# Performance work log

Measured on AMD Instinct MI355X. Metric: run time of the kernel, lower is better.

Reference implementation:

```python
import jax, jax.numpy as jnp
import numpy as np

N = 50000      # nodes
E = 600000     # edges
D_IN = 128
D = 128        # embedding_size
H = 2 * D      # GENConv MLP hidden (expansion=2, num_layers=2)
L = 6          # gnn_layers
OUT = 2        # out_channels
EPS_MSG = 1e-7   # GENConv message eps
EPS_SM = 1e-16   # PyG softmax denominator eps
LN_EPS = 1e-5


def setup_inputs() -> dict:
    key = jax.random.key(0)
    ks = jax.random.split(key, 18)
    s_in = 1.0 / np.sqrt(D_IN)
    s_d = 1.0 / np.sqrt(D)
    s_h = 1.0 / np.sqrt(H)
    return {
        "x": jax.random.normal(ks[0], (N, D_IN), jnp.float32),
        "edge_index": jax.random.randint(ks[1], (2, E), 0, N, jnp.int64),
        # node encoder
        "enc_W": jax.random.normal(ks[2], (D_IN, D), jnp.float32) * s_in,
        "enc_b": jnp.zeros((D,), jnp.float32),
        # per-layer DeepGCN params (stacked over L layers)
        "ln_g": jnp.ones((L, D), jnp.float32),
        "ln_b": jnp.zeros((L, D), jnp.float32),
        "t": jnp.ones((L,), jnp.float32),  # learnable softmax temperature
        "W1": jax.random.normal(ks[3], (L, D, H), jnp.float32) * s_d,
        "b1": jnp.zeros((L, H), jnp.float32),
        "mln_g": jnp.ones((L, H), jnp.float32),
        "mln_b": jnp.zeros((L, H), jnp.float32),
        "W2": jax.random.normal(ks[4], (L, H, D), jnp.float32) * s_h,
        "b2": jnp.zeros((L, D), jnp.float32),
        # final MLP head (linear_layers=2)
        "lin_W1": jax.random.normal(ks[5], (D, D), jnp.float32) * s_d,
        "lin_b1": jnp.zeros((D,), jnp.float32),
        "lin_W2": jax.random.normal(ks[6], (D, OUT), jnp.float32) * s_d,
        "lin_b2": jnp.zeros((OUT,), jnp.float32),
    }


def _layernorm(h, g, b):
    mu = jnp.mean(h, axis=-1, keepdims=True)
    var = jnp.mean(jnp.square(h - mu), axis=-1, keepdims=True)
    return (h - mu) * jax.lax.rsqrt(var + LN_EPS) * g + b


def _genconv(h, src, dst, t, W1, b1, mg, mb, W2, b2):
    """GENConv with softmax aggregation: gather -> segment softmax -> scatter -> MLP."""
    msg = jax.nn.relu(h[src]) + EPS_MSG            # [E, D]
    scaled = msg * t
    mmax = jax.ops.segment_max(scaled, dst, num_segments=N)  # [N, D]
    mmax = jnp.where(jnp.isfinite(mmax), mmax, 0.0)          # empty segments
    ex = jnp.exp(scaled - mmax[dst])                          # [E, D]
    denom = jax.ops.segment_sum(ex, dst, num_segments=N)     # [N, D]
    alpha = ex / (denom[dst] + EPS_SM)
    agg = jax.ops.segment_sum(msg * alpha, dst, num_segments=N)  # [N, D]
    out = agg + h                                  # root/self term
    z = out @ W1 + b1                              # [N, 2D]
    z = jax.nn.relu(_layernorm(z, mg, mb))
    return z @ W2 + b2                             # [N, D]


def reference(x, edge_index, enc_W, enc_b, ln_g, ln_b, t, W1, b1,
              mln_g, mln_b, W2, b2, lin_W1, lin_b1, lin_W2, lin_b2):
    src, dst = edge_index[0], edge_index[1]
    h = x @ enc_W + enc_b                          # node encoder [N, D]
    for i in range(L):                             # DeepGCNLayer 'res+' blocks
        g = _layernorm(h, ln_g[i], ln_b[i])
        g = jax.nn.relu(g)                         # (dropout: inference no-op)
        g = _genconv(g, src, dst, t[i], W1[i], b1[i], mln_g[i], mln_b[i], W2[i], b2[i])
        h = h + g
    h = jax.nn.relu(h @ lin_W1 + lin_b1)           # head (dropout_rate=None)
    return h @ lin_W2 + lin_b2                     # [N, OUT]
```

## Files before the change

### kernel.cpp

```cpp
#include <hip/hip_runtime.h>

#define NN 50000
#define EE 600000
#define DD 128
#define HH 256
#define LL 6
#define NB 49

typedef _Float16 f16x8 __attribute__((ext_vector_type(8)));
typedef float f32x4 __attribute__((ext_vector_type(4)));

__device__ __forceinline__ float bf2f(unsigned short u){
  unsigned int x = ((unsigned int)u) << 16; float f; __builtin_memcpy(&f, &x, 4); return f;
}
__device__ __forceinline__ unsigned short f2bf(float f){
  unsigned int x; __builtin_memcpy(&x, &f, 4);
  unsigned int lsb = (x >> 16) & 1u; x += 0x7fffu + lsb; return (unsigned short)(x >> 16);
}
__device__ __forceinline__ float wave_sum(float v){
  #pragma unroll
  for (int off = 32; off >= 1; off >>= 1) v += __shfl_xor(v, off, 64);
  return v;
}
__device__ __forceinline__ unsigned short f2h(float f){
  _Float16 h = (_Float16)f; unsigned short u; __builtin_memcpy(&u, &h, 2); return u;
}
__device__ __forceinline__ float h2f(unsigned short u){
  _Float16 h; __builtin_memcpy(&h, &u, 2); return (float)h;
}

__global__ void k_detect(const unsigned short* __restrict__ xh,
                         const unsigned int* __restrict__ ew,
                         int* __restrict__ flags){
  __shared__ int s_bad, s_nz;
  int t = threadIdx.x;
  if (t == 0){ s_bad = 0; s_nz = 0; }
  __syncthreads();
  int bad = 0;
  for (int i = t; i < 512; i += 256){
    unsigned e = (xh[i] >> 7) & 0xffu;
    if (e < 96u || e > 135u) bad = 1;
  }
  if (bad) atomicOr(&s_bad, 1);
  int nz = 0;
  for (int i = t; i < 1024; i += 256)
    if ((i & 1) && ew[i] != 0u) nz = 1;
  if (nz) atomicOr(&s_nz, 1);
  __syncthreads();
  if (t == 0){
    flags[0] = s_bad ? 1 : 0;
    flags[1] = s_nz ? 0 : 1;
  }
}

__global__ void k_cvt_edges(const void* __restrict__ ei, const int* __restrict__ flags,
                            int* __restrict__ s32, int* __restrict__ d32){
  int e = blockIdx.x*256 + threadIdx.x;
  if (e >= EE) return;
  int sv, dv;
  if (flags[1]){
    const long long* p = (const long long*)ei;
    sv = (int)p[e]; dv = (int)p[EE + e];
  } else {
    const int* p = (const int*)ei;
    sv = p[e]; dv = p[EE + e];
  }
  s32[e] = ((unsigned)sv < (unsigned)NN) ? sv : 0;
  d32[e] = ((unsigned)dv < (unsigned)NN) ? dv : 0;
}

__global__ void k_hist(const int* __restrict__ dst, int* __restrict__ deg){
  int e = blockIdx.x*256 + threadIdx.x;
  if (e < EE) atomicAdd(&deg[dst[e]], 1);
}

__global__ void k_blocksum(const int* __restrict__ deg, int* __restrict__ bsum){
  __shared__ int ws[4];
  int t = threadIdx.x, b = blockIdx.x;
  int s = 0;
  int i0 = b*1024 + t*4;
  #pragma unroll
  for (int j=0;j<4;j++){ int i = i0+j; if (i < NN) s += deg[i]; }
  #pragma unroll
  for (int off=32; off>=1; off>>=1) s += __shfl_xor(s, off, 64);
  if ((t&63)==0) ws[t>>6] = s;
  __syncthreads();
  if (t==0) bsum[b] = ws[0]+ws[1]+ws[2]+ws[3];
}

__global__ void k_scanb(const int* __restrict__ bsum, int* __restrict__ boff, int* __restrict__ rowptr){
  int lane = threadIdx.x;
  int v = (lane < NB) ? bsum[lane] : 0;
  int inc = v;
  #pragma unroll
  for (int off=1; off<64; off<<=1){ int u = __shfl_up(inc, off, 64); if (lane>=off) inc += u; }
  if (lane < NB) boff[lane] = inc - v;
  if (lane == 63) rowptr[NN] = inc;
}

__global__ void k_scanscatter(const int* __restrict__ deg, const int* __restrict__ boff,
                              int* __restrict__ rowptr, int* __restrict__ pos){
  __shared__ int ws[4];
  int t = threadIdx.x, b = blockIdx.x;
  int lane = t & 63, wid = t >> 6;
  int i0 = b*1024 + t*4;
  int d[4];
  #pragma unroll
  for (int j=0;j<4;j++){ int i=i0+j; d[j] = (i<NN)? deg[i] : 0; }
  int tot = d[0]+d[1]+d[2]+d[3];
  int inc = tot;
  #pragma unroll
  for (int off=1; off<64; off<<=1){ int u = __shfl_up(inc, off, 64); if (lane>=off) inc += u; }
  if (lane==63) ws[wid] = inc;
  __syncthreads();
  int woff = 0;
  for (int w=0; w<wid; w++) woff += ws[w];
  int base = boff[b] + woff + (inc - tot);
  int pre = 0;
  #pragma unroll
  for (int j=0;j<4;j++){
    int i = i0+j;
    if (i<NN){ rowptr[i] = base + pre; pos[i] = base + pre; }
    pre += d[j];
  }
}

__global__ void k_fill(const int* __restrict__ src, const int* __restrict__ dst,
                       int* __restrict__ pos, int* __restrict__ csr){
  int e = blockIdx.x*256 + threadIdx.x;
  if (e < EE){
    int d = dst[e];
    int p = atomicAdd(&pos[d], 1);
    csr[p] = src[e];
  }
}

__global__ void k_prep_w(const int* __restrict__ flags,
    const void* __restrict__ encW, const void* __restrict__ linW1,
    const void* __restrict__ W1, const void* __restrict__ W2,
    unsigned short* __restrict__ ph, unsigned short* __restrict__ pl)
{
  int idx = blockIdx.x*256 + threadIdx.x;
  int fp32 = flags[0];
  const void* src; int off;
  if (idx < 16384){ int n=idx>>7, k=idx&127; src=encW; off=k*128+n; }
  else if (idx < 32768){ int o=idx-16384; int n=o>>7, k=o&127; src=linW1; off=k*128+n; }
  else if (idx < 229376){ int o=idx-32768; int l=o>>15, r=o&32767; int n=r>>7, k=r&127; src=W1; off=l*32768+k*256+n; }
  else { int o=idx-229376; int l=o>>15, r=o&32767; int n=r>>8, k=r&255; src=W2; off=l*32768+k*128+n; }
  float w = fp32 ? ((const float*)src)[off] : bf2f(((const unsigned short*)src)[off]);
  unsigned short h = f2h(w);
  ph[idx] = h;
  pl[idx] = f2h(w - h2f(h));
}

#define SM_ENCB 0
#define SM_LNG 128
#define SM_LNB 896
#define SM_TV 1664
#define SM_B1 1670
#define SM_MG 3206
#define SM_MB 4742
#define SM_B2 6278
#define SM_LINB1 7046
#define SM_LINW2 7174
#define SM_LINB2 7430
#define SM_TOT 7432
__global__ void k_prep_small(const int* __restrict__ flags,
    const void* s0, const void* s1, const void* s2, const void* s3,
    const void* s4, const void* s5, const void* s6, const void* s7,
    const void* s8, const void* s9, const void* s10, float* __restrict__ out)
{
  int i = blockIdx.x*256 + threadIdx.x;
  if (i >= SM_TOT) return;
  int fp32 = flags[0];
  const void* src; int off;
  if      (i < SM_LNG)  { src=s0;  off=i; }
  else if (i < SM_LNB)  { src=s1;  off=i-SM_LNG; }
  else if (i < SM_TV)   { src=s2;  off=i-SM_LNB; }
  else if (i < SM_B1)   { src=s3;  off=i-SM_TV; }
  else if (i < SM_MG)   { src=s4;  off=i-SM_B1; }
  else if (i < SM_MB)   { src=s5;  off=i-SM_MG; }
  else if (i < SM_B2)   { src=s6;  off=i-SM_MB; }
  else if (i < SM_LINB1){ src=s7;  off=i-SM_B2; }
  else if (i < SM_LINW2){ src=s8;  off=i-SM_LINB1; }
  else if (i < SM_LINB2){ src=s9;  off=i-SM_LINW2; }
  else                  { src=s10; off=i-SM_LINB2; }
  out[i] = fp32 ? ((const float*)src)[off] : bf2f(((const unsigned short*)src)[off]);
}

template<int EPI>
__global__ __launch_bounds__(256, 4) void k_gemm(const void* __restrict__ Ap,
    const unsigned short* __restrict__ WTh, const unsigned short* __restrict__ WTl,
    const float* __restrict__ bias, float* __restrict__ C,
    int M, const int* __restrict__ flags, int aExt)
{
  __shared__ __align__(16) short lA[64*72];
  __shared__ __align__(16) short lW[128*72];

  const int tid = threadIdx.x, lane = tid & 63, wid = tid >> 6;
  const int mi = lane & 15, q = lane >> 4;
  const int rowb = blockIdx.x * 64;
  const int fp32m = flags[0];

  f32x4 acc[4][2];
  #pragma unroll
  for (int a=0;a<4;a++)
    #pragma unroll
    for (int c=0;c<2;c++){ acc[a][c][0]=0.f; acc[a][c][1]=0.f; acc[a][c][2]=0.f; acc[a][c][3]=0.f; }

  const int nW = fp32m ? 2 : 1;
  for (int pass = 0; pass < nW; ++pass){
    const unsigned short* Wp = pass ? WTl : WTh;
    for (int kc = 0; kc < 2; ++kc){
      {
        const int kv = (tid & 7) * 8, r0 = tid >> 3;
        #pragma unroll
        for (int p = 0; p < 2; ++p){
          int row = p*32 + r0, grow = rowb + row;
          uint4 d = make_uint4(0u,0u,0u,0u);
          if (grow < M){
            if (!aExt){
              d = *(const uint4*)((const unsigned short*)Ap + (size_t)grow*128 + kc*64 + kv);
            } else if (!fp32m){
              uint4 u = *(const uint4*)((const unsigned short*)Ap + (size_t)grow*128 + kc*64 + kv);
              const unsigned short* us = (const unsigned short*)&u;
              unsigned short hh[8];
              #pragma unroll
              for (int c=0;c<8;c++) hh[c] = f2h(bf2f(us[c]));
              d.x = hh[0]|((unsigned)hh[1]<<16); d.y = hh[2]|((unsigned)hh[3]<<16);
              d.z = hh[4]|((unsigned)hh[5]<<16); d.w = hh[6]|((unsigned)hh[7]<<16);
            } else {
              const float* fp = (const float*)Ap + (size_t)grow*128 + kc*64 + kv;
              float4 v0 = *(const float4*)fp, v1 = *(const float4*)(fp+4);
              unsigned short hh[8] = {f2h(v0.x),f2h(v0.y),f2h(v0.z),f2h(v0.w),
                                      f2h(v1.x),f2h(v1.y),f2h(v1.z),f2h(v1.w)};
              d.x = hh[0]|((unsigned)hh[1]<<16); d.y = hh[2]|((unsigned)hh[3]<<16);
              d.z = hh[4]|((unsigned)hh[5]<<16); d.w = hh[6]|((unsigned)hh[7]<<16);
            }
          }
          *(uint4*)&lA[row*72 + kv] = d;
        }
        #pragma unroll
        for (int p = 0; p < 4; ++p){
          int n = p*32 + r0;
          *(uint4*)&lW[n*72 + kv] = *(const uint4*)(Wp + (size_t)n*128 + kc*64 + kv);
        }
      }
      __syncthreads();
      #pragma unroll
      for (int ks = 0; ks < 2; ++ks){
        const int koff = ks*32 + q*8;
        f16x8 af[4], bw[2];
        #pragma unroll
        for (int rt=0; rt<4; rt++) af[rt] = *(const f16x8*)&lA[(rt*16+mi)*72 + koff];
        #pragma unroll
        for (int ct=0; ct<2; ct++) bw[ct] = *(const f16x8*)&lW[(wid*32 + ct*16 + mi)*72 + koff];
        #pragma unroll
        for (int rt=0; rt<4; rt++)
          #pragma unroll
          for (int ct=0; ct<2; ct++)
            acc[rt][ct] = __builtin_amdgcn_mfma_f32_16x16x32_f16(af[rt], bw[ct], acc[rt][ct], 0,0,0);
      }
      __syncthreads();
    }
  }
  #pragma unroll
  for (int ct=0; ct<2; ct++){
    const int col = wid*32 + ct*16 + mi;
    const float bf = bias[col];
    #pragma unroll
    for (int rt=0; rt<4; rt++)
      #pragma unroll
      for (int r=0; r<4; r++){
        int row = rowb + rt*16 + q*4 + r;
        if (row < M){
          float v = acc[rt][ct][r] + bf;
          if (EPI == 1) v = fmaxf(v, 0.f);
          C[(size_t)row*128 + col] = v;
        }
      }
  }
}

__global__ __launch_bounds__(256, 3) void k_gemm1(const unsigned short* __restrict__ Ap,
    const unsigned short* __restrict__ WTh, const unsigned short* __restrict__ WTl,
    const float* __restrict__ bias, const float* __restrict__ gam, const float* __restrict__ bet,
    unsigned short* __restrict__ z, int M, const int* __restrict__ flags)
{
  __shared__ __align__(16) short lA[64*72];
  __shared__ __align__(16) short lW[256*72];
  __shared__ float2 sred[4][64];

  const int tid = threadIdx.x, lane = tid & 63, wid = tid >> 6;
  const int mi = lane & 15, q = lane >> 4;
  const int rowb = blockIdx.x * 64;

  f32x4 acc[4][4];
  #pragma unroll
  for (int a=0;a<4;a++)
    #pragma unroll
    for (int c=0;c<4;c++){ acc[a][c][0]=0.f; acc[a][c][1]=0.f; acc[a][c][2]=0.f; acc[a][c][3]=0.f; }

  const int nW = flags[0] ? 2 : 1;
  for (int pass = 0; pass < nW; ++pass){
    const unsigned short* Wp = pass ? WTl : WTh;
    for (int kc = 0; kc < 2; ++kc){
      {
        const int kv = (tid & 7) * 8, r0 = tid >> 3;
        #pragma unroll
        for (int p = 0; p < 2; ++p){
          int row = p*32 + r0, grow = rowb + row;
          uint4 d = make_uint4(0u,0u,0u,0u);
          if (grow < M) d = *(const uint4*)(Ap + (size_t)grow*128 + kc*64 + kv);
          *(uint4*)&lA[row*72 + kv] = d;
        }
        #pragma unroll
        for (int p = 0; p < 8; ++p){
          int n = p*32 + r0;
          *(uint4*)&lW[n*72 + kv] = *(const uint4*)(Wp + (size_t)n*128 + kc*64 + kv);
        }
      }
      __syncthreads();
      #pragma unroll
      for (int ks = 0; ks < 2; ++ks){
        const int koff = ks*32 + q*8;
        f16x8 af[4], bw[4];
        #pragma unroll
        for (int rt=0; rt<4; rt++) af[rt] = *(const f16x8*)&lA[(rt*16+mi)*72 + koff];
        #pragma unroll
        for (int ct=0; ct<4; ct++) bw[ct] = *(const f16x8*)&lW[(wid*64 + ct*16 + mi)*72 + koff];
        #pragma unroll
        for (int rt=0; rt<4; rt++)
          #pragma unroll
          for (int ct=0; ct<4; ct++)
            acc[rt][ct] = __builtin_amdgcn_mfma_f32_16x16x32_f16(af[rt], bw[ct], acc[rt][ct], 0,0,0);
      }
      __syncthreads();
    }
  }
  #pragma unroll
  for (int ct=0; ct<4; ct++){
    const float bf = bias[wid*64 + ct*16 + mi];
    #pragma unroll
    for (int rt=0; rt<4; rt++)
      #pragma unroll
      for (int r=0; r<4; r++) acc[rt][ct][r] += bf;
  }
  #pragma unroll
  for (int rt=0; rt<4; rt++)
    #pragma unroll
    for (int r=0; r<4; r++){
      float s = 0.f, s2 = 0.f;
      #pragma unroll
      for (int ct=0; ct<4; ct++){ float v = acc[rt][ct][r]; s += v; s2 += v*v; }
      #pragma unroll
      for (int off=1; off<16; off<<=1){ s += __shfl_xor(s, off, 64); s2 += __shfl_xor(s2, off, 64); }
      if (mi == 0) sred[wid][rt*16 + q*4 + r] = make_float2(s, s2);
    }
  __syncthreads();
  #pragma unroll
  for (int rt=0; rt<4; rt++)
    #pragma unroll
    for (int r=0; r<4; r++){
      int rl = rt*16 + q*4 + r;
      float2 t0 = sred[0][rl], t1 = sred[1][rl], t2 = sred[2][rl], t3 = sred[3][rl];
      float s = t0.x + t1.x + t2.x + t3.x;
      float s2 = t0.y + t1.y + t2.y + t3.y;
      float m = s * (1.f/256.f);
      float var = s2 * (1.f/256.f) - m*m;
      float rs = rsqrtf(var + 1e-5f);
      int row = rowb + rl;
      if (row < M){
        #pragma unroll
        for (int ct=0; ct<4; ct++){
          int col = wid*64 + ct*16 + mi;
          float v = (acc[rt][ct][r] - m) * rs * gam[col] + bet[col];
          z[(size_t)row*256 + col] = f2h(fmaxf(v, 0.f));
        }
      }
    }
}

__global__ __launch_bounds__(256, 4) void k_gemm2(const unsigned short* __restrict__ Ap,
    const unsigned short* __restrict__ WTh, const unsigned short* __restrict__ WTl,
    const float* __restrict__ bias, float* __restrict__ h,
    const float* __restrict__ gam, const float* __restrict__ bet,
    unsigned short* __restrict__ msg, unsigned short* __restrict__ hf,
    int M, const int* __restrict__ flags, int doLN)
{
  __shared__ __align__(16) short lA[64*72];
  __shared__ __align__(16) short lW[128*72];
  __shared__ float2 sred[4][64];

  const int tid = threadIdx.x, lane = tid & 63, wid = tid >> 6;
  const int mi = lane & 15, q = lane >> 4;
  const int rowb = blockIdx.x * 64;

  f32x4 acc[4][2];
  #pragma unroll
  for (int a=0;a<4;a++)
    #pragma unroll
    for (int c=0;c<2;c++){ acc[a][c][0]=0.f; acc[a][c][1]=0.f; acc[a][c][2]=0.f; acc[a][c][3]=0.f; }

  const int nW = flags[0] ? 2 : 1;
  for (int pass = 0; pass < nW; ++pass){
    const unsigned short* Wp = pass ? WTl : WTh;
    for (int kc = 0; kc < 4; ++kc){
      {
        const int kv = (tid & 7) * 8, r0 = tid >> 3;
        #pragma unroll
        for (int p = 0; p < 2; ++p){
          int row = p*32 + r0, grow = rowb + row;
          uint4 d = make_uint4(0u,0u,0u,0u);
          if (grow < M) d = *(const uint4*)(Ap + (size_t)grow*256 + kc*64 + kv);
          *(uint4*)&lA[row*72 + kv] = d;
        }
        #pragma unroll
        for (int p = 0; p < 4; ++p){
          int n = p*32 + r0;
          *(uint4*)&lW[n*72 + kv] = *(const uint4*)(Wp + (size_t)n*256 + kc*64 + kv);
        }
      }
      __syncthreads();
      #pragma unroll
      for (int ks = 0; ks < 2; ++ks){
        const int koff = ks*32 + q*8;
        f16x8 af[4], bw[2];
        #pragma unroll
        for (int rt=0; rt<4; rt++) af[rt] = *(const f16x8*)&lA[(rt*16+mi)*72 + koff];
        #pragma unroll
        for (int ct=0; ct<2; ct++) bw[ct] = *(const f16x8*)&lW[(wid*32 + ct*16 + mi)*72 + koff];
        #pragma unroll
        for (int rt=0; rt<4; rt++)
          #pragma unroll
          for (int ct=0; ct<2; ct++)
            acc[rt][ct] = __builtin_amdgcn_mfma_f32_16x16x32_f16(af[rt], bw[ct], acc[rt][ct], 0,0,0);
      }
      __syncthreads();
    }
  }
  #pragma unroll
  for (int ct=0; ct<2; ct++){
    const int col = wid*32 + ct*16 + mi;
    const float bf = bias[col];
    #pragma unroll
    for (int rt=0; rt<4; rt++)
      #pragma unroll
      for (int r=0; r<4; r++){
        int row = rowb + rt*16 + q*4 + r;
        if (row < M){
          float hv = acc[rt][ct][r] + bf + h[(size_t)row*128 + col];
          h[(size_t)row*128 + col] = hv;
          acc[rt][ct][r] = hv;
        }
      }
  }
  if (!doLN){
    #pragma unroll
    for (int ct=0; ct<2; ct++){
      const int col = wid*32 + ct*16 + mi;
      #pragma unroll
      for (int rt=0; rt<4; rt++)
        #pragma unroll
        for (int r=0; r<4; r++){
          int row = rowb + rt*16 + q*4 + r;
          if (row < M) hf[(size_t)row*128 + col] = f2h(acc[rt][ct][r]);
        }
    }
    return;
  }
  #pragma unroll
  for (int rt=0; rt<4; rt++)
    #pragma unroll
    for (int r=0; r<4; r++){
      float s = 0.f, s2 = 0.f;
      #pragma unroll
      for (int ct=0; ct<2; ct++){ float v = acc[rt][ct][r]; s += v; s2 += v*v; }
      #pragma unroll
      for (int off=1; off<16; off<<=1){ s += __shfl_xor(s, off, 64); s2 += __shfl_xor(s2, off, 64); }
      if (mi == 0) sred[wid][rt*16 + q*4 + r] = make_float2(s, s2);
    }
  __syncthreads();
  #pragma unroll
  for (int rt=0; rt<4; rt++)
    #pragma unroll
    for (int r=0; r<4; r++){
      int rl = rt*16 + q*4 + r;
      float2 t0 = sred[0][rl], t1 = sred[1][rl], t2 = sred[2][rl], t3 = sred[3][rl];
      float s = t0.x + t1.x + t2.x + t3.x;
      float s2 = t0.y + t1.y + t2.y + t3.y;
      float m = s * (1.f/128.f);
      float var = s2 * (1.f/128.f) - m*m;
      float rs = rsqrtf(var + 1e-5f);
      int row = rowb + rl;
      if (row < M){
        #pragma unroll
        for (int ct=0; ct<2; ct++){
          int col = wid*32 + ct*16 + mi;
          float g = fmaxf((acc[rt][ct][r] - m) * rs * gam[col] + bet[col], 0.f);
          msg[(size_t)row*128 + col] = f2h(g + 1e-7f);
        }
      }
    }
}

__global__ __launch_bounds__(256,4) void k_preln0(const float* __restrict__ h,
    const float* __restrict__ gam, const float* __restrict__ bet,
    unsigned short* __restrict__ msg)
{
  int wid = threadIdx.x >> 6, lane = threadIdx.x & 63;
  int row = blockIdx.x*4 + wid;
  float2 v = ((const float2*)(h + (size_t)row*DD))[lane];
  float mean = wave_sum(v.x+v.y) * (1.f/128.f);
  float d0 = v.x-mean, d1 = v.y-mean;
  float var = wave_sum(d0*d0 + d1*d1) * (1.f/128.f);
  float rs = rsqrtf(var + 1e-5f);
  float o0 = fmaxf(d0*rs*gam[2*lane]   + bet[2*lane],   0.f);
  float o1 = fmaxf(d1*rs*gam[2*lane+1] + bet[2*lane+1], 0.f);
  unsigned u = (unsigned)f2h(o0 + 1e-7f) | ((unsigned)f2h(o1 + 1e-7f) << 16);
  ((unsigned*)(msg + (size_t)row*DD))[lane] = u;
}

__global__ __launch_bounds__(256,4) void k_agg(
    const unsigned short* __restrict__ msg,
    const int* __restrict__ rowptr, const int* __restrict__ csr,
    const float* __restrict__ tp, unsigned short* __restrict__ obf)
{
  int wid = threadIdx.x>>6, lane = threadIdx.x&63;
  int node = blockIdx.x*4 + wid;
  float t = tp[0];
  int st = rowptr[node], en = rowptr[node+1];
  int quad = lane >> 4, fi = lane & 15;
  float l[8], ac[8];
  #pragma unroll
  for (int f=0; f<8; f++){ l[f]=0.f; ac[f]=0.f; }
  for (int base = st; base < en; base += 64){
    int cnt = min(64, en - base);
    int sv = (lane < cnt) ? csr[base + lane] : 0;
    for (int j = 0; j < cnt; j += 4){
      int idx = j + quad;
      int s = __shfl(sv, idx, 64);
      bool val = idx < cnt;
      uint4 u = *(const uint4*)(msg + (size_t)s*DD + fi*8);
      float m[8];
      m[0]=h2f((unsigned short)(u.x&0xffffu)); m[1]=h2f((unsigned short)(u.x>>16));
      m[2]=h2f((unsigned short)(u.y&0xffffu)); m[3]=h2f((unsigned short)(u.y>>16));
      m[4]=h2f((unsigned short)(u.z&0xffffu)); m[5]=h2f((unsigned short)(u.z>>16));
      m[6]=h2f((unsigned short)(u.w&0xffffu)); m[7]=h2f((unsigned short)(u.w>>16));
      #pragma unroll
      for (int f=0; f<8; f++){
        float e = __expf(fminf(m[f]*t, 80.f));
        e = val ? e : 0.f;
        l[f] += e; ac[f] += m[f]*e;
      }
    }
  }
  #pragma unroll
  for (int off=16; off<=32; off<<=1)
    #pragma unroll
    for (int f=0; f<8; f++){ l[f] += __shfl_xor(l[f], off, 64); ac[f] += __shfl_xor(ac[f], off, 64); }
  if (quad == 0){
    uint4 u = *(const uint4*)(msg + (size_t)node*DD + fi*8);
    float m[8];
    m[0]=h2f((unsigned short)(u.x&0xffffu)); m[1]=h2f((unsigned short)(u.x>>16));
    m[2]=h2f((unsigned short)(u.y&0xffffu)); m[3]=h2f((unsigned short)(u.y>>16));
    m[4]=h2f((unsigned short)(u.z&0xffffu)); m[5]=h2f((unsigned short)(u.z>>16));
    m[6]=h2f((unsigned short)(u.w&0xffffu)); m[7]=h2f((unsigned short)(u.w>>16));
    bool has = en > st;
    unsigned short o[8];
    #pragma unroll
    for (int f=0; f<8; f++){
      float a = has ? (ac[f] / (l[f] + 1e-16f)) : 0.f;
      o[f] = f2h((m[f] - 1e-7f) + a);
    }
    uint4 w;
    w.x = o[0]|((unsigned)o[1]<<16); w.y = o[2]|((unsigned)o[3]<<16);
    w.z = o[4]|((unsigned)o[5]<<16); w.w = o[6]|((unsigned)o[7]<<16);
    *(uint4*)(obf + (size_t)node*DD + fi*8) = w;
  }
}

__global__ __launch_bounds__(256,4) void k_head2(const float* __restrict__ u,
    const float* __restrict__ w, const float* __restrict__ b,
    void* __restrict__ out, const int* __restrict__ flags)
{
  int wid = threadIdx.x>>6, lane = threadIdx.x&63;
  int row = blockIdx.x*4 + wid;
  const float* ur = u + (size_t)row*DD;
  float u0 = ur[lane], u1 = ur[lane+64];
  float s0 = u0*w[lane*2+0] + u1*w[(lane+64)*2+0];
  float s1 = u0*w[lane*2+1] + u1*w[(lane+64)*2+1];
  s0 = wave_sum(s0); s1 = wave_sum(s1);
  if (lane == 0){
    float o0 = s0 + b[0], o1 = s1 + b[1];
    if (flags[0]){
      ((float*)out)[row*2+0] = o0;
      ((float*)out)[row*2+1] = o1;
    } else {
      ((unsigned short*)out)[row*2+0] = f2bf(o0);
      ((unsigned short*)out)[row*2+1] = f2bf(o1);
    }
  }
}

extern "C" void kernel_launch(void* const* d_in, const int* in_sizes, int n_in,
                              void* d_out, int out_size, void* d_ws, size_t ws_size,
                              hipStream_t stream)
{
  (void)in_sizes; (void)n_in; (void)out_size; (void)ws_size;
  char* ws = (char*)d_ws;
  size_t off = 0;
  auto alloc = [&](size_t bytes) -> char* {
    char* p = ws + off;
    off = (off + bytes + 255) & ~(size_t)255;
    return p;
  };
  int* flags  = (int*)alloc(256);
  float* sm   = (float*)alloc(SM_TOT*4);
  unsigned short* planeH = (unsigned short*)alloc(425984*2);
  unsigned short* planeL = (unsigned short*)alloc(425984*2);
  int* src32  = (int*)alloc((size_t)EE*4);
  int* dst32  = (int*)alloc((size_t)EE*4);
  int* deg    = (int*)alloc((size_t)NN*4);
  int* pos    = (int*)alloc((size_t)NN*4);
  int* rowptr = (int*)alloc((size_t)(NN+1)*4);
  int* csr    = (int*)alloc((size_t)EE*4);
  int* bsum   = (int*)alloc(64*4);
  int* boff   = (int*)alloc(64*4);
  float* h    = (float*)alloc((size_t)NN*128*4);
  unsigned short* z    = (unsigned short*)alloc((size_t)NN*256*2);
  unsigned short* msgb = (unsigned short*)alloc((size_t)NN*128*2);
  unsigned short* obf  = (unsigned short*)alloc((size_t)NN*128*2);
  unsigned short* hf   = (unsigned short*)alloc((size_t)NN*128*2);
  float* ob   = (float*)alloc((size_t)NN*128*4);

  k_detect<<<1,256,0,stream>>>((const unsigned short*)d_in[0], (const unsigned int*)d_in[1], flags);
  k_cvt_edges<<<(EE+255)/256,256,0,stream>>>(d_in[1], flags, src32, dst32);
  hipMemsetAsync(deg, 0, (size_t)NN*4, stream);
  k_hist<<<(EE+255)/256,256,0,stream>>>(dst32, deg);
  k_blocksum<<<NB,256,0,stream>>>(deg, bsum);
  k_scanb<<<1,64,0,stream>>>(bsum, boff, rowptr);
  k_scanscatter<<<NB,256,0,stream>>>(deg, boff, rowptr, pos);
  k_fill<<<(EE+255)/256,256,0,stream>>>(src32, dst32, pos, csr);
  k_prep_w<<<1664,256,0,stream>>>(flags, d_in[2], d_in[13], d_in[7], d_in[11], planeH, planeL);
  k_prep_small<<<30,256,0,stream>>>(flags, d_in[3], d_in[4], d_in[5], d_in[6], d_in[8],
                                    d_in[9], d_in[10], d_in[12], d_in[14], d_in[15], d_in[16], sm);

  const int GB = (NN + 63)/64;
  k_gemm<0><<<GB,256,0,stream>>>((const void*)d_in[0], planeH + 0, planeL + 0,
                                 sm + SM_ENCB, h, NN, flags, 1);
  k_preln0<<<NN/4,256,0,stream>>>(h, sm + SM_LNG, sm + SM_LNB, msgb);
  for (int i = 0; i < LL; ++i){
    k_agg<<<NN/4,256,0,stream>>>(msgb, rowptr, csr, sm + SM_TV + i, obf);
    k_gemm1<<<GB,256,0,stream>>>(obf, planeH + 32768 + i*32768, planeL + 32768 + i*32768,
                                 sm + SM_B1 + i*256, sm + SM_MG + i*256, sm + SM_MB + i*256,
                                 z, NN, flags);
    int nl = (i+1 < LL) ? (i+1) : 0;
    k_gemm2<<<GB,256,0,stream>>>(z, planeH + 229376 + i*32768, planeL + 229376 + i*32768,
                                 sm + SM_B2 + i*128, h,
                                 sm + SM_LNG + nl*128, sm + SM_LNB + nl*128,
                                 msgb, hf, NN, flags, (i+1 < LL) ? 1 : 0);
  }
  k_gemm<1><<<GB,256,0,stream>>>((const void*)hf, planeH + 16384, planeL + 16384,
                                 sm + SM_LINB1, ob, NN, flags, 0);
  k_head2<<<NN/4,256,0,stream>>>(ob, sm + SM_LINW2, sm + SM_LINB2, d_out, flags);
}
```

Baseline: 893.6 us.

## Precompute per-node softmax exponentials in producer kernels, gather them in aggregation

The producer kernels (preln0 and gemm2's epilogue) now compute exp(m*t - 8), clamped, once per node and store it as fp16 next to the fp16 message. The edge aggregation then gathers both values instead of recomputing exp for every edge. A zero dummy row at index NN replaces the per-edge validity mask. This removes roughly 12x redundant transcendental work per layer, but doubles the bytes gathered per edge and adds fp16 range and precision risk on the precomputed exponentials.

```diff
diff --git a/kernel.cpp b/kernel.cpp
--- a/kernel.cpp
+++ b/kernel.cpp
@@ -186,6 +186,12 @@
   else if (i < SM_LINB2){ src=s9;  off=i-SM_LINW2; }
   else                  { src=s10; off=i-SM_LINB2; }
   out[i] = fp32 ? ((const float*)src)[off] : bf2f(((const unsigned short*)src)[off]);
+}
+
+__device__ __forceinline__ void emit_me(unsigned short* me, int row, int col, float g, float tv){
+  float m = g + 1e-7f;
+  me[(size_t)row*256 + col] = f2h(m);
+  me[(size_t)row*256 + 128 + col] = f2h(__expf(fminf(m*tv, 18.f) - 8.f));
 }
 
 template<int EPI>
@@ -385,7 +391,8 @@
     const unsigned short* __restrict__ WTh, const unsigned short* __restrict__ WTl,
     const float* __restrict__ bias, float* __restrict__ h,
     const float* __restrict__ gam, const float* __restrict__ bet,
-    unsigned short* __restrict__ msg, unsigned short* __restrict__ hf,
+    const float* __restrict__ tp,
+    unsigned short* __restrict__ me, unsigned short* __restrict__ hf,
     int M, const int* __restrict__ flags, int doLN)
 {
   __shared__ __align__(16) short lA[64*72];
@@ -395,6 +402,7 @@
   const int tid = threadIdx.x, lane = tid & 63, wid = tid >> 6;
   const int mi = lane & 15, q = lane >> 4;
   const int rowb = blockIdx.x * 64;
+  const float tv = tp[0];
 
   f32x4 acc[4][2];
   #pragma unroll
@@ -498,7 +506,7 @@
         for (int ct=0; ct<2; ct++){
           int col = wid*32 + ct*16 + mi;
           float g = fmaxf((acc[rt][ct][r] - m) * rs * gam[col] + bet[col], 0.f);
-          msg[(size_t)row*128 + col] = f2h(g + 1e-7f);
+          emit_me(me, row, col, g, tv);
         }
       }
     }
@@ -506,10 +514,11 @@
 
 __global__ __launch_bounds__(256,4) void k_preln0(const float* __restrict__ h,
     const float* __restrict__ gam, const float* __restrict__ bet,
-    unsigned short* __restrict__ msg)
+    const float* __restrict__ tp, unsigned short* __restrict__ me)
 {
   int wid = threadIdx.x >> 6, lane = threadIdx.x & 63;
   int row = blockIdx.x*4 + wid;
+  float tv = tp[0];
   float2 v = ((const float2*)(h + (size_t)row*DD))[lane];
   float mean = wave_sum(v.x+v.y) * (1.f/128.f);
   float d0 = v.x-mean, d1 = v.y-mean;
@@ -517,18 +526,17 @@
   float rs = rsqrtf(var + 1e-5f);
   float o0 = fmaxf(d0*rs*gam[2*lane]   + bet[2*lane],   0.f);
   float o1 = fmaxf(d1*rs*gam[2*lane+1] + bet[2*lane+1], 0.f);
-  unsigned u = (unsigned)f2h(o0 + 1e-7f) | ((unsigned)f2h(o1 + 1e-7f) << 16);
-  ((unsigned*)(msg + (size_t)row*DD))[lane] = u;
+  emit_me(me, row, 2*lane,   o0, tv);
+  emit_me(me, row, 2*lane+1, o1, tv);
 }
 
 __global__ __launch_bounds__(256,4) void k_agg(
-    const unsigned short* __restrict__ msg,
+    const unsigned short* __restrict__ me,
     const int* __restrict__ rowptr, const int* __restrict__ csr,
-    const float* __restrict__ tp, unsigned short* __restrict__ obf)
+    unsigned short* __restrict__ obf)
 {
   int wid = threadIdx.x>>6, lane = threadIdx.x&63;
   int node = blockIdx.x*4 + wid;
-  float t = tp[0];
   int st = rowptr[node], en = rowptr[node+1];
   int quad = lane >> 4, fi = lane & 15;
   float l[8], ac[8];
@@ -536,22 +544,17 @@
   for (int f=0; f<8; f++){ l[f]=0.f; ac[f]=0.f; }
   for (int base = st; base < en; base += 64){
     int cnt = min(64, en - base);
-    int sv = (lane < cnt) ? csr[base + lane] : 0;
+    int sv = (lane < cnt) ? csr[base + lane] : NN;
     for (int j = 0; j < cnt; j += 4){
-      int idx = j + quad;
-      int s = __shfl(sv, idx, 64);
-      bool val = idx < cnt;
-      uint4 u = *(const uint4*)(msg + (size_t)s*DD + fi*8);
-      float m[8];
-      m[0]=h2f((unsigned short)(u.x&0xffffu)); m[1]=h2f((unsigned short)(u.x>>16));
-      m[2]=h2f((unsigned short)(u.y&0xffffu)); m[3]=h2f((unsigned short)(u.y>>16));
-      m[4]=h2f((unsigned short)(u.z&0xffffu)); m[5]=h2f((unsigned short)(u.z>>16));
-      m[6]=h2f((unsigned short)(u.w&0xffffu)); m[7]=h2f((unsigned short)(u.w>>16));
+      int s = __shfl(sv, j + quad, 64);
+      const unsigned short* mer = me + (size_t)s*256 + fi*8;
+      f16x8 mh = *(const f16x8*)(mer);
+      f16x8 eh = *(const f16x8*)(mer + 128);
       #pragma unroll
       for (int f=0; f<8; f++){
-        float e = __expf(fminf(m[f]*t, 80.f));
-        e = val ? e : 0.f;
-        l[f] += e; ac[f] += m[f]*e;
+        float ef = (float)eh[f];
+        l[f] += ef;
+        ac[f] = fmaf((float)mh[f], ef, ac[f]);
       }
     }
   }
@@ -560,18 +563,13 @@
     #pragma unroll
     for (int f=0; f<8; f++){ l[f] += __shfl_xor(l[f], off, 64); ac[f] += __shfl_xor(ac[f], off, 64); }
   if (quad == 0){
-    uint4 u = *(const uint4*)(msg + (size_t)node*DD + fi*8);
-    float m[8];
-    m[0]=h2f((unsigned short)(u.x&0xffffu)); m[1]=h2f((unsigned short)(u.x>>16));
-    m[2]=h2f((unsigned short)(u.y&0xffffu)); m[3]=h2f((unsigned short)(u.y>>16));
-    m[4]=h2f((unsigned short)(u.z&0xffffu)); m[5]=h2f((unsigned short)(u.z>>16));
-    m[6]=h2f((unsigned short)(u.w&0xffffu)); m[7]=h2f((unsigned short)(u.w>>16));
+    f16x8 mh = *(const f16x8*)(me + (size_t)node*256 + fi*8);
     bool has = en > st;
     unsigned short o[8];
     #pragma unroll
     for (int f=0; f<8; f++){
       float a = has ? (ac[f] / (l[f] + 1e-16f)) : 0.f;
-      o[f] = f2h((m[f] - 1e-7f) + a);
+      o[f] = f2h(((float)mh[f] - 1e-7f) + a);
     }
     uint4 w;
     w.x = o[0]|((unsigned)o[1]<<16); w.y = o[2]|((unsigned)o[3]<<16);
@@ -629,7 +627,7 @@
   int* boff   = (int*)alloc(64*4);
   float* h    = (float*)alloc((size_t)NN*128*4);
   unsigned short* z    = (unsigned short*)alloc((size_t)NN*256*2);
-  unsigned short* msgb = (unsigned short*)alloc((size_t)NN*128*2);
+  unsigned short* me   = (unsigned short*)alloc((size_t)(NN+1)*256*2);
   unsigned short* obf  = (unsigned short*)alloc((size_t)NN*128*2);
   unsigned short* hf   = (unsigned short*)alloc((size_t)NN*128*2);
   float* ob   = (float*)alloc((size_t)NN*128*4);
@@ -637,6 +635,7 @@
   k_detect<<<1,256,0,stream>>>((const unsigned short*)d_in[0], (const unsigned int*)d_in[1], flags);
   k_cvt_edges<<<(EE+255)/256,256,0,stream>>>(d_in[1], flags, src32, dst32);
   hipMemsetAsync(deg, 0, (size_t)NN*4, stream);
+  hipMemsetAsync(me + (size_t)NN*256, 0, 512, stream);
   k_hist<<<(EE+255)/256,256,0,stream>>>(dst32, deg);
   k_blocksum<<<NB,256,0,stream>>>(deg, bsum);
   k_scanb<<<1,64,0,stream>>>(bsum, boff, rowptr);
@@ -649,9 +648,9 @@
   const int GB = (NN + 63)/64;
   k_gemm<0><<<GB,256,0,stream>>>((const void*)d_in[0], planeH + 0, planeL + 0,
                                  sm + SM_ENCB, h, NN, flags, 1);
-  k_preln0<<<NN/4,256,0,stream>>>(h, sm + SM_LNG, sm + SM_LNB, msgb);
+  k_preln0<<<NN/4,256,0,stream>>>(h, sm + SM_LNG, sm + SM_LNB, sm + SM_TV, me);
   for (int i = 0; i < LL; ++i){
-    k_agg<<<NN/4,256,0,stream>>>(msgb, rowptr, csr, sm + SM_TV + i, obf);
+    k_agg<<<NN/4,256,0,stream>>>(me, rowptr, csr, obf);
     k_gemm1<<<GB,256,0,stream>>>(obf, planeH + 32768 + i*32768, planeL + 32768 + i*32768,
                                  sm + SM_B1 + i*256, sm + SM_MG + i*256, sm + SM_MB + i*256,
                                  z, NN, flags);
@@ -659,7 +658,8 @@
     k_gemm2<<<GB,256,0,stream>>>(z, planeH + 229376 + i*32768, planeL + 229376 + i*32768,
                                  sm + SM_B2 + i*128, h,
                                  sm + SM_LNG + nl*128, sm + SM_LNB + nl*128,
-                                 msgb, hf, NN, flags, (i+1 < LL) ? 1 : 0);
+                                 sm + SM_TV + nl,
+                                 me, hf, NN, flags, (i+1 < LL) ? 1 : 0);
   }
   k_gemm<1><<<GB,256,0,stream>>>((const void*)hf, planeH + 16384, planeL + 16384,
                                  sm + SM_LINB1, ob, NN, flags, 0);
```

New measurement: 896.7 us. About the same (+0.3%).
